# Kernel tuning notes

Hardware: AMD Instinct MI355X
Metric: run time of the kernel (lower is better)

## Reference

```python
import jax, jax.numpy as jnp
import numpy as np

HIDDEN = 2048
INTER = 4096
NUM_EXPERTS = 8
TOP_K = 4
BATCH, SEQ = 2, 2048
TOKENS = BATCH * SEQ


def setup_inputs() -> dict:
    key = jax.random.key(0)
    k_x, k_rw, k_tw, k_te, k_gu, k_dn = jax.random.split(key, 6)
    x = jax.random.normal(k_x, (BATCH, SEQ, HIDDEN), dtype=jnp.float32)
    # full router weights (passed through but unused by this patched forward)
    weights = jax.random.uniform(k_rw, (TOKENS, NUM_EXPERTS), dtype=jnp.float32)
    tw = jax.random.uniform(k_tw, (TOKENS, TOP_K), dtype=jnp.float32)
    top_weights = tw / jnp.sum(tw, axis=-1, keepdims=True)  # softmax-like, renormalize=False downstream
    top_experts = jax.random.randint(k_te, (TOKENS, TOP_K), 0, NUM_EXPERTS, dtype=jnp.int64)
    scale_gu = 1.0 / np.sqrt(HIDDEN)
    scale_dn = 1.0 / np.sqrt(INTER)
    gate_up_weights = jax.random.normal(k_gu, (NUM_EXPERTS, 2 * INTER, HIDDEN), dtype=jnp.float32) * scale_gu
    down_weights = jax.random.normal(k_dn, (NUM_EXPERTS, HIDDEN, INTER), dtype=jnp.float32) * scale_dn
    return {
        'x': x,
        'weights': weights,
        'top_weights': top_weights,
        'top_experts': top_experts,
        'gate_up_weights': gate_up_weights,
        'down_weights': down_weights,
    }


def _fused_moe(xf, gate_up_weights, down_weights, top_weights, top_experts):
    """xf: [T, D]. Dense per-expert loop (scan over experts), masked combine.

    Matches fused_moe(renormalize=False): out[t] = sum_k top_weights[t,k] * expert_{top_experts[t,k]}(x[t])
    expert(x) = (silu(x @ Wg^T) * (x @ Wu^T)) @ Wd^T with [Wg; Wu] = gate_up.
    """
    E = gate_up_weights.shape[0]

    def step(out, inp):
        w_gu, w_d, e = inp
        # per-token combine coefficient for this expert (0 if not routed)
        coef = jnp.sum(jnp.where(top_experts == e, top_weights, 0.0), axis=-1)  # [T]
        h = xf @ w_gu.T                       # [T, 2*INTER]
        gate, up = jnp.split(h, 2, axis=-1)
        act = jax.nn.silu(gate) * up          # [T, INTER]
        o = act @ w_d.T                       # [T, D]
        return out + coef[:, None] * o, None

    out, _ = jax.lax.scan(step, jnp.zeros_like(xf),
                          (gate_up_weights, down_weights, jnp.arange(E, dtype=jnp.int64)))
    return out


def reference(x, weights, top_weights, top_experts, gate_up_weights, down_weights):
    B, S, D = x.shape
    xf = x.reshape(-1, D)  # flatten(0, 1)
    out = _fused_moe(xf, gate_up_weights, down_weights, top_weights, top_experts)
    return out.reshape(B, S, D)  # unflatten(0, (-1, q_len))
```

## Files before the change

kernel.cpp:

```cpp
#include <hip/hip_runtime.h>
#include <stdint.h>

#define T_TOKENS 4096
#define D_HID    2048
#define D_INT    4096
#define N_EXP    8
#define TOPK     4
#define NFLAT    (T_TOKENS*TOPK)
#define BMT      256
#define MAXPAD   (NFLAT + N_EXP*BMT)
#define MT2      (MAXPAD/BMT)

#define OFF_PTOK 0ull
#define OFF_PWT  73728ull
#define OFF_CNT  147456ull
#define OFF_TOFF 147712ull
#define OFF_SEG  155904ull
#define OFF_XB   262144ull
#define OFF_ACT  17039360ull
#define OFF_W    168034304ull

typedef float f32x4  __attribute__((ext_vector_type(4)));
typedef short bf16x8 __attribute__((ext_vector_type(8)));

__device__ __forceinline__ unsigned short f2bf(float f) {
    unsigned int u = __float_as_uint(f);
    u += 0x7fffu + ((u >> 16) & 1u);
    return (unsigned short)(u >> 16);
}

__device__ __forceinline__ void gload_lds16(const void* g, void* l) {
    __builtin_amdgcn_global_load_lds((const __attribute__((address_space(1))) void*)g,
                                     (__attribute__((address_space(3))) void*)l,
                                     16, 0, 0);
}

__device__ __forceinline__ int xcd_logical(int hw, int nwg) {
    int q = nwg >> 3, r = nwg & 7;
    int xc = hw & 7, sl = hw >> 3;
    return (xc < r ? xc * (q + 1) : r * (q + 1) + (xc - r) * q) + sl;
}

__global__ void k_prep(const float* __restrict__ x, unsigned short* __restrict__ xb,
                       float* __restrict__ out) {
    int i = blockIdx.x * 256 + threadIdx.x;
    float4 v = ((const float4*)x)[i];
    ushort4 h;
    h.x = f2bf(v.x); h.y = f2bf(v.y); h.z = f2bf(v.z); h.w = f2bf(v.w);
    ((ushort4*)xb)[i] = h;
    ((float4*)out)[i] = make_float4(0.f, 0.f, 0.f, 0.f);
}

__global__ void k_cast(const float* __restrict__ src, unsigned short* __restrict__ dst) {
    size_t i = (size_t)blockIdx.x * 256 + threadIdx.x;
    float4 v = ((const float4*)src)[i];
    ushort4 h;
    h.x = f2bf(v.x); h.y = f2bf(v.y); h.z = f2bf(v.z); h.w = f2bf(v.w);
    ((ushort4*)dst)[i] = h;
}

__global__ void k_count(const int* __restrict__ te, int* __restrict__ counts,
                        int* __restrict__ toff) {
    int e = blockIdx.x, t = threadIdx.x;
    int cnt = 0;
    int base = t * 64;
    for (int i = 0; i < 64; i++) cnt += (te[base + i] == e);
    __shared__ int s[256];
    s[t] = cnt; __syncthreads();
    int incl = cnt;
    for (int off = 1; off < 256; off <<= 1) {
        int tmp = (t >= off) ? s[t - off] : 0;
        __syncthreads();
        incl += tmp; s[t] = incl;
        __syncthreads();
    }
    toff[e * 256 + t] = incl - cnt;
    if (t == 255) counts[e] = incl;
}

__global__ void k_fill(const int* __restrict__ te, const float* __restrict__ tw,
                       const int* __restrict__ counts, const int* __restrict__ toff,
                       int* __restrict__ ptok, float* __restrict__ pwt, int* __restrict__ seg) {
    int e = blockIdx.x, t = threadIdx.x;
    int segs[9]; int a = 0;
    #pragma unroll
    for (int j = 0; j < 8; j++) { segs[j] = a; a += (counts[j] + BMT - 1) & ~(BMT - 1); }
    segs[8] = a;
    if (e == 0 && t == 0) { for (int j = 0; j < 9; j++) seg[j] = segs[j]; }
    int base = segs[e] + toff[e * 256 + t];
    int rank = 0;
    for (int i = t * 64; i < (t + 1) * 64; i++) {
        if (te[i] == e) { ptok[base + rank] = i >> 2; pwt[base + rank] = tw[i]; rank++; }
    }
    int cnt = counts[e], pc = (cnt + BMT - 1) & ~(BMT - 1);
    for (int i = cnt + t; i < pc; i += 256) { ptok[segs[e] + i] = -1; pwt[segs[e] + i] = 0.f; }
}


#define KSTEP(VMS) \
  asm volatile("s_waitcnt vmcnt(" VMS ")" ::: "memory"); \
  __builtin_amdgcn_s_barrier(); \
  __builtin_amdgcn_sched_barrier(0); \
  { \
    const char* pT = ldsc + (cb << 15); \
    bf16x8 af[8], bf[4]; \
    _Pragma("unroll") for (int m_ = 0; m_ < 8; ++m_) \
        af[m_] = *(const bf16x8*)(pT + a_off + m_ * 1024); \
    _Pragma("unroll") for (int n_ = 0; n_ < 4; ++n_) \
        bf[n_] = *(const bf16x8*)(pT + b_off + n_ * 1024); \
    asm volatile("s_waitcnt lgkmcnt(0)" ::: "memory"); \
    __builtin_amdgcn_sched_barrier(0); \
    __builtin_amdgcn_s_barrier(); \
    __builtin_amdgcn_s_setprio(1); \
    _Pragma("unroll") for (int m_ = 0; m_ < 8; ++m_) \
      _Pragma("unroll") for (int n_ = 0; n_ < 4; ++n_) \
        acc[m_][n_] = __builtin_amdgcn_mfma_f32_16x16x32_bf16(af[m_], bf[n_], acc[m_][n_], 0, 0, 0); \
    __builtin_amdgcn_s_setprio(0); \
    cb = (cb + 1) & 3; \
  }

__global__ void __launch_bounds__(512, 2)
k_g1(const unsigned short* __restrict__ xb, const unsigned short* __restrict__ wgu_b,
     const int* __restrict__ ptok, const int* __restrict__ seg,
     unsigned short* __restrict__ act) {
    extern __shared__ char smem[];
    char* ldsw = smem; const char* ldsc = smem;
    int logical = xcd_logical(blockIdx.x, 2304);
    int nb = logical / MT2, mb = logical % MT2;
    if (mb * BMT >= seg[8]) return;
    int e = 0;
    #pragma unroll
    for (int j = 1; j < 8; ++j) if (seg[j] <= mb * BMT) e = j;
    int tid = threadIdx.x, w = tid >> 6, l = tid & 63;
    int wr = w >> 2, wc = w & 3;

    int g = (l & 3) ^ ((l >> 3) & 3);
    int r0 = w * 16 + (l >> 2), r1 = 128 + r0;
    int t0 = ptok[mb * BMT + r0]; if (t0 < 0) t0 = 0;
    int t1 = ptok[mb * BMT + r1]; if (t1 < 0) t1 = 0;
    const char* pa0 = (const char*)xb + (size_t)t0 * 4096 + g * 16;
    const char* pa1 = (const char*)xb + (size_t)t1 * 4096 + g * 16;
    int wcr0 = r0 >> 6, j0 = r0 & 63;
    int wcr1 = r1 >> 6, j1 = r1 & 63;
    int gr0 = (j0 < 32) ? (nb * 128 + wcr0 * 32 + j0) : (D_INT + nb * 128 + wcr0 * 32 + j0 - 32);
    int gr1 = (j1 < 32) ? (nb * 128 + wcr1 * 32 + j1) : (D_INT + nb * 128 + wcr1 * 32 + j1 - 32);
    const char* wbase = (const char*)wgu_b + (size_t)e * 8192 * 4096;
    const char* pb0 = wbase + (size_t)gr0 * 4096 + g * 16;
    const char* pb1 = wbase + (size_t)gr1 * 4096 + g * 16;
    int dA0 = w * 1024, dA1 = 8192 + w * 1024;
    int dB0 = 16384 + w * 1024, dB1 = 24576 + w * 1024;
    int sb = 0;
    auto STAGE = [&]() {
        char* d = ldsw + (sb << 15);
        gload_lds16(pa0, d + dA0); gload_lds16(pa1, d + dA1);
        gload_lds16(pb0, d + dB0); gload_lds16(pb1, d + dB1);
        pa0 += 64; pa1 += 64; pb0 += 64; pb1 += 64;
        sb = (sb + 1) & 3;
    };

    int off_frag = (l & 15) * 64 + ((((l >> 4)) ^ (((l & 15) >> 1) & 3)) << 4);
    int a_off = wr * 8192 + off_frag;
    int b_off = 16384 + wc * 4096 + off_frag;

    f32x4 acc[8][4];
    #pragma unroll
    for (int m = 0; m < 8; ++m)
        #pragma unroll
        for (int n = 0; n < 4; ++n) acc[m][n] = (f32x4){0.f, 0.f, 0.f, 0.f};

    int cb = 0;
    STAGE(); STAGE(); STAGE();
    for (int kt = 0; kt < 61; ++kt) { STAGE(); KSTEP("12") }
    KSTEP("8") KSTEP("4") KSTEP("0")

    int mbase = mb * BMT;
    #pragma unroll
    for (int m = 0; m < 8; ++m) {
        int rowl = wr * 128 + m * 16 + (l >> 4) * 4;
        #pragma unroll
        for (int np = 0; np < 2; ++np) {
            int col = nb * 128 + wc * 32 + np * 16 + (l & 15);
            #pragma unroll
            for (int r = 0; r < 4; ++r) {
                float gv = acc[m][np][r], uv = acc[m][np + 2][r];
                float av = gv / (1.f + __expf(-gv)) * uv;
                act[(size_t)(mbase + rowl + r) * D_INT + col] = f2bf(av);
            }
        }
    }
}

__global__ void __launch_bounds__(512, 2)
k_g2(const unsigned short* __restrict__ act, const unsigned short* __restrict__ wd_b,
     const int* __restrict__ ptok, const float* __restrict__ pwt,
     const int* __restrict__ seg, float* __restrict__ out) {
    extern __shared__ char smem[];
    char* ldsw = smem; const char* ldsc = smem;
    int logical = xcd_logical(blockIdx.x, 1152);
    int pair = logical / MT2, mb = logical % MT2;
    int nb = pair >> 1, ks = pair & 1;
    if (mb * BMT >= seg[8]) return;
    int e = 0;
    #pragma unroll
    for (int j = 1; j < 8; ++j) if (seg[j] <= mb * BMT) e = j;
    int tid = threadIdx.x, w = tid >> 6, l = tid & 63;
    int wr = w >> 2, wc = w & 3;
    int koff = ks * 4096;

    int g = (l & 3) ^ ((l >> 3) & 3);
    int r0 = w * 16 + (l >> 2), r1 = 128 + r0;
    const char* pa0 = (const char*)act + (size_t)(mb * BMT + r0) * 8192 + koff + g * 16;
    const char* pa1 = (const char*)act + (size_t)(mb * BMT + r1) * 8192 + koff + g * 16;
    const char* wbase = (const char*)wd_b + (size_t)e * D_HID * 8192;
    const char* pb0 = wbase + (size_t)(nb * 256 + r0) * 8192 + koff + g * 16;
    const char* pb1 = wbase + (size_t)(nb * 256 + r1) * 8192 + koff + g * 16;
    int dA0 = w * 1024, dA1 = 8192 + w * 1024;
    int dB0 = 16384 + w * 1024, dB1 = 24576 + w * 1024;
    int sb = 0;
    auto STAGE = [&]() {
        char* d = ldsw + (sb << 15);
        gload_lds16(pa0, d + dA0); gload_lds16(pa1, d + dA1);
        gload_lds16(pb0, d + dB0); gload_lds16(pb1, d + dB1);
        pa0 += 64; pa1 += 64; pb0 += 64; pb1 += 64;
        sb = (sb + 1) & 3;
    };

    int off_frag = (l & 15) * 64 + ((((l >> 4)) ^ (((l & 15) >> 1) & 3)) << 4);
    int a_off = wr * 8192 + off_frag;
    int b_off = 16384 + wc * 4096 + off_frag;

    f32x4 acc[8][4];
    #pragma unroll
    for (int m = 0; m < 8; ++m)
        #pragma unroll
        for (int n = 0; n < 4; ++n) acc[m][n] = (f32x4){0.f, 0.f, 0.f, 0.f};

    int cb = 0;
    STAGE(); STAGE(); STAGE();
    for (int kt = 0; kt < 61; ++kt) { STAGE(); KSTEP("12") }
    KSTEP("8") KSTEP("4") KSTEP("0")

    #pragma unroll
    for (int m = 0; m < 8; ++m) {
        int rowl = wr * 128 + m * 16 + (l >> 4) * 4;
        #pragma unroll
        for (int r = 0; r < 4; ++r) {
            int p = mb * BMT + rowl + r;
            int tok = ptok[p];
            float wt = pwt[p];
            if (tok >= 0) {
                #pragma unroll
                for (int n = 0; n < 4; ++n) {
                    int col = nb * 256 + wc * 64 + n * 16 + (l & 15);
                    unsafeAtomicAdd(&out[(size_t)tok * D_HID + col], wt * acc[m][n][r]);
                }
            }
        }
    }
}

extern "C" void kernel_launch(void* const* d_in, const int* in_sizes, int n_in,
                              void* d_out, int out_size, void* d_ws, size_t ws_size,
                              hipStream_t stream) {
    const float* x   = (const float*)d_in[0];
    const float* tw  = (const float*)d_in[2];
    const int*   te  = (const int*)d_in[3];
    const float* wgu = (const float*)d_in[4];
    const float* wd  = (const float*)d_in[5];
    float* out = (float*)d_out;
    char*  ws  = (char*)d_ws;

    int*   ptok   = (int*)(ws + OFF_PTOK);
    float* pwt    = (float*)(ws + OFF_PWT);
    int*   counts = (int*)(ws + OFF_CNT);
    int*   toff   = (int*)(ws + OFF_TOFF);
    int*   seg    = (int*)(ws + OFF_SEG);
    unsigned short* xb  = (unsigned short*)(ws + OFF_XB);
    unsigned short* act = (unsigned short*)(ws + OFF_ACT);
    unsigned short* w_b = (unsigned short*)(ws + OFF_W);

    hipFuncSetAttribute((const void*)k_g1, hipFuncAttributeMaxDynamicSharedMemorySize, 131072);
    hipFuncSetAttribute((const void*)k_g2, hipFuncAttributeMaxDynamicSharedMemorySize, 131072);

    k_prep<<<8192, 256, 0, stream>>>(x, xb, out);
    k_count<<<N_EXP, 256, 0, stream>>>(te, counts, toff);
    k_fill<<<N_EXP, 256, 0, stream>>>(te, tw, counts, toff, ptok, pwt, seg);

    k_cast<<<131072, 256, 0, stream>>>(wgu, w_b);
    k_g1<<<2304, 512, 131072, stream>>>(xb, w_b, ptok, seg, act);
    k_cast<<<65536, 256, 0, stream>>>(wd, w_b);
    k_g2<<<1152, 512, 131072, stream>>>(act, w_b, ptok, pwt, seg, out);
}
```

Baseline: 1.268 ms.

## Split MFMA k-step into two halves interleaving LDS reads, use grid-stride casts

```diff
diff --git a/kernel.cpp b/kernel.cpp
--- a/kernel.cpp
+++ b/kernel.cpp
@@ -43,20 +43,23 @@
 
 __global__ void k_prep(const float* __restrict__ x, unsigned short* __restrict__ xb,
                        float* __restrict__ out) {
-    int i = blockIdx.x * 256 + threadIdx.x;
-    float4 v = ((const float4*)x)[i];
-    ushort4 h;
-    h.x = f2bf(v.x); h.y = f2bf(v.y); h.z = f2bf(v.z); h.w = f2bf(v.w);
-    ((ushort4*)xb)[i] = h;
-    ((float4*)out)[i] = make_float4(0.f, 0.f, 0.f, 0.f);
-}
-
-__global__ void k_cast(const float* __restrict__ src, unsigned short* __restrict__ dst) {
-    size_t i = (size_t)blockIdx.x * 256 + threadIdx.x;
-    float4 v = ((const float4*)src)[i];
-    ushort4 h;
-    h.x = f2bf(v.x); h.y = f2bf(v.y); h.z = f2bf(v.z); h.w = f2bf(v.w);
-    ((ushort4*)dst)[i] = h;
+    const int N4 = T_TOKENS * D_HID / 4;
+    for (int i = blockIdx.x * 256 + threadIdx.x; i < N4; i += 2048 * 256) {
+        float4 v = ((const float4*)x)[i];
+        ushort4 h;
+        h.x = f2bf(v.x); h.y = f2bf(v.y); h.z = f2bf(v.z); h.w = f2bf(v.w);
+        ((ushort4*)xb)[i] = h;
+        ((float4*)out)[i] = make_float4(0.f, 0.f, 0.f, 0.f);
+    }
+}
+
+__global__ void k_cast(const float* __restrict__ src, unsigned short* __restrict__ dst, int n4) {
+    for (int i = blockIdx.x * 256 + threadIdx.x; i < n4; i += 2048 * 256) {
+        float4 v = ((const float4*)src)[i];
+        ushort4 h;
+        h.x = f2bf(v.x); h.y = f2bf(v.y); h.z = f2bf(v.z); h.w = f2bf(v.w);
+        ((ushort4*)dst)[i] = h;
+    }
 }
 
 __global__ void k_count(const int* __restrict__ te, int* __restrict__ counts,
@@ -97,24 +100,35 @@
 }
 
 
-#define KSTEP(VMS) \
+#define MFMA4(MI, AF) \
+    _Pragma("unroll") for (int n_ = 0; n_ < 4; ++n_) \
+        acc[MI][n_] = __builtin_amdgcn_mfma_f32_16x16x32_bf16(AF, bf[n_], acc[MI][n_], 0, 0, 0);
+
+#define GBODY(VMS) \
   asm volatile("s_waitcnt vmcnt(" VMS ")" ::: "memory"); \
   __builtin_amdgcn_s_barrier(); \
   __builtin_amdgcn_sched_barrier(0); \
   { \
     const char* pT = ldsc + (cb << 15); \
-    bf16x8 af[8], bf[4]; \
-    _Pragma("unroll") for (int m_ = 0; m_ < 8; ++m_) \
-        af[m_] = *(const bf16x8*)(pT + a_off + m_ * 1024); \
+    bf16x8 bf[4], af[4], ag[4]; \
     _Pragma("unroll") for (int n_ = 0; n_ < 4; ++n_) \
         bf[n_] = *(const bf16x8*)(pT + b_off + n_ * 1024); \
+    _Pragma("unroll") for (int m_ = 0; m_ < 4; ++m_) \
+        af[m_] = *(const bf16x8*)(pT + a_off + m_ * 1024); \
+    __builtin_amdgcn_s_barrier(); \
+    asm volatile("s_waitcnt lgkmcnt(0)" ::: "memory"); \
+    __builtin_amdgcn_sched_barrier(0); \
+    __builtin_amdgcn_s_setprio(1); \
+    MFMA4(0, af[0]) MFMA4(1, af[1]) MFMA4(2, af[2]) MFMA4(3, af[3]) \
+    __builtin_amdgcn_s_setprio(0); \
+    __builtin_amdgcn_sched_barrier(0); \
+    _Pragma("unroll") for (int m_ = 0; m_ < 4; ++m_) \
+        ag[m_] = *(const bf16x8*)(pT + a_off + 4096 + m_ * 1024); \
     asm volatile("s_waitcnt lgkmcnt(0)" ::: "memory"); \
     __builtin_amdgcn_sched_barrier(0); \
     __builtin_amdgcn_s_barrier(); \
     __builtin_amdgcn_s_setprio(1); \
-    _Pragma("unroll") for (int m_ = 0; m_ < 8; ++m_) \
-      _Pragma("unroll") for (int n_ = 0; n_ < 4; ++n_) \
-        acc[m_][n_] = __builtin_amdgcn_mfma_f32_16x16x32_bf16(af[m_], bf[n_], acc[m_][n_], 0, 0, 0); \
+    MFMA4(4, ag[0]) MFMA4(5, ag[1]) MFMA4(6, ag[2]) MFMA4(7, ag[3]) \
     __builtin_amdgcn_s_setprio(0); \
     cb = (cb + 1) & 3; \
   }
@@ -140,10 +154,11 @@
     int t1 = ptok[mb * BMT + r1]; if (t1 < 0) t1 = 0;
     const char* pa0 = (const char*)xb + (size_t)t0 * 4096 + g * 16;
     const char* pa1 = (const char*)xb + (size_t)t1 * 4096 + g * 16;
-    int wcr0 = r0 >> 6, j0 = r0 & 63;
-    int wcr1 = r1 >> 6, j1 = r1 & 63;
-    int gr0 = (j0 < 32) ? (nb * 128 + wcr0 * 32 + j0) : (D_INT + nb * 128 + wcr0 * 32 + j0 - 32);
-    int gr1 = (j1 < 32) ? (nb * 128 + wcr1 * 32 + j1) : (D_INT + nb * 128 + wcr1 * 32 + j1 - 32);
+    int j0 = r0 & 63, j1 = r1 & 63;
+    int gr0 = (j0 < 32) ? (nb * 128 + (r0 >> 6) * 32 + j0)
+                        : (D_INT + nb * 128 + (r0 >> 6) * 32 + j0 - 32);
+    int gr1 = (j1 < 32) ? (nb * 128 + (r1 >> 6) * 32 + j1)
+                        : (D_INT + nb * 128 + (r1 >> 6) * 32 + j1 - 32);
     const char* wbase = (const char*)wgu_b + (size_t)e * 8192 * 4096;
     const char* pb0 = wbase + (size_t)gr0 * 4096 + g * 16;
     const char* pb1 = wbase + (size_t)gr1 * 4096 + g * 16;
@@ -170,8 +185,8 @@
 
     int cb = 0;
     STAGE(); STAGE(); STAGE();
-    for (int kt = 0; kt < 61; ++kt) { STAGE(); KSTEP("12") }
-    KSTEP("8") KSTEP("4") KSTEP("0")
+    for (int G = 0; G < 61; ++G) { STAGE(); GBODY("12") }
+    GBODY("8") GBODY("4") GBODY("0")
 
     int mbase = mb * BMT;
     #pragma unroll
@@ -237,8 +252,8 @@
 
     int cb = 0;
     STAGE(); STAGE(); STAGE();
-    for (int kt = 0; kt < 61; ++kt) { STAGE(); KSTEP("12") }
-    KSTEP("8") KSTEP("4") KSTEP("0")
+    for (int G = 0; G < 61; ++G) { STAGE(); GBODY("12") }
+    GBODY("8") GBODY("4") GBODY("0")
 
     #pragma unroll
     for (int m = 0; m < 8; ++m) {
@@ -282,12 +297,12 @@
     hipFuncSetAttribute((const void*)k_g1, hipFuncAttributeMaxDynamicSharedMemorySize, 131072);
     hipFuncSetAttribute((const void*)k_g2, hipFuncAttributeMaxDynamicSharedMemorySize, 131072);
 
-    k_prep<<<8192, 256, 0, stream>>>(x, xb, out);
+    k_prep<<<2048, 256, 0, stream>>>(x, xb, out);
     k_count<<<N_EXP, 256, 0, stream>>>(te, counts, toff);
     k_fill<<<N_EXP, 256, 0, stream>>>(te, tw, counts, toff, ptok, pwt, seg);
 
-    k_cast<<<131072, 256, 0, stream>>>(wgu, w_b);
+    k_cast<<<2048, 256, 0, stream>>>(wgu, w_b, 33554432);
     k_g1<<<2304, 512, 131072, stream>>>(xb, w_b, ptok, seg, act);
-    k_cast<<<65536, 256, 0, stream>>>(wd, w_b);
+    k_cast<<<2048, 256, 0, stream>>>(wd, w_b, 16777216);
     k_g2<<<1152, 512, 131072, stream>>>(act, w_b, ptok, pwt, seg, out);
 }
```

Measured after the change: 1.325 ms. +4.4%, slower.
